# Kernel tuning notes

Hardware: AMD Instinct MI355X
Metric: run time of the kernel (lower is better)

Reference implementation:

```python
import jax, jax.numpy as jnp
import numpy as np

B, E, S, H, HD, M, MLP = 8, 1024, 2000, 16, 64, 10, 4096
EPS = 1e-5

def setup_inputs() -> dict:
    key = jax.random.key(0)
    ks = jax.random.split(key, 12)
    s = lambda k, shape, sc: jax.random.normal(k, shape, dtype=jnp.float32) * sc
    return {
        'X': s(ks[0], (B, E, S), 1.0),
        'Wq': s(ks[1], (H, HD, E), E ** -0.5), 'bq': s(ks[2], (H, HD), 0.02),
        'Wk': s(ks[3], (H, HD, E), E ** -0.5), 'bk': s(ks[4], (H, HD), 0.02),
        'Wv': s(ks[5], (H, HD, E), E ** -0.5), 'bv': s(ks[6], (H, HD), 0.02),
        'g1': jnp.ones((E,), jnp.float32), 'be1': jnp.zeros((E,), jnp.float32),
        'W1': s(ks[7], (MLP, E), E ** -0.5), 'b1': s(ks[8], (MLP,), 0.02),
        'W2': s(ks[9], (E, MLP), MLP ** -0.5), 'b2': s(ks[10], (E,), 0.02),
        'g2': jnp.ones((E,), jnp.float32), 'be2': jnp.zeros((E,), jnp.float32),
    }

def iterative_inv(K, n_iter=6):
    I = jnp.eye(K.shape[-1], dtype=K.dtype)
    # global (over all batch/head) max row-sum * max col-sum init, as in Nystromformer
    V = K.swapaxes(-1, -2) / (jnp.max(jnp.sum(jnp.abs(K), axis=-2)) * jnp.max(jnp.sum(jnp.abs(K), axis=-1)))
    for _ in range(n_iter):
        KV = K @ V
        V = 0.25 * V @ (13.0 * I - KV @ (15.0 * I - KV @ (7.0 * I - KV)))
    return V

def layer_norm(x, g, b):
    mu = jnp.mean(x, axis=-1, keepdims=True)
    var = jnp.var(x, axis=-1, keepdims=True)
    return (x - mu) * jax.lax.rsqrt(var + EPS) * g + b

def reference(X, Wq, bq, Wk, bk, Wv, bv, g1, be1, W1, b1, W2, b2, g2, be2):
    x = jnp.swapaxes(X, 1, 2)  # (B, S, E)
    # per-head projections (stacked): (B, H, S, HD)
    Q = jnp.einsum('bse,hde->bhsd', x, Wq) + bq[None, :, None, :]
    K = jnp.einsum('bse,hde->bhsd', x, Wk) + bk[None, :, None, :]
    V = jnp.einsum('bse,hde->bhsd', x, Wv) + bv[None, :, None, :]
    scale = 1.0 / np.sqrt(np.sqrt(HD)).astype(np.float32)
    Q = Q * scale
    K = K * scale
    # landmarks: mean over segments of length S//M -> (B, H, M, HD)
    Ql = Q.reshape(B, H, M, S // M, HD).mean(axis=-2)
    Kl = K.reshape(B, H, M, S // M, HD).mean(axis=-2)
    k1 = jax.nn.softmax(jnp.einsum('bhsd,bhmd->bhsm', Q, Kl), axis=-1)   # (B,H,S,M)
    k2 = jax.nn.softmax(jnp.einsum('bhnd,bhmd->bhnm', Ql, Kl), axis=-1)  # (B,H,M,M)
    k3 = jax.nn.softmax(jnp.einsum('bhmd,bhsd->bhms', Ql, K), axis=-1)   # (B,H,M,S)
    attn = (k1 @ iterative_inv(k2)) @ (k3 @ V)  # (B,H,S,HD)
    attn = jnp.swapaxes(attn, 1, 2).reshape(B, S, E)
    h = layer_norm(attn, g1, be1)
    h = jax.nn.gelu(h @ W1.T + b1, approximate=False)
    h = h @ W2.T + b2
    h = layer_norm(h, g2, be2)
    return jnp.swapaxes(h, 2, 1)  # (B, E, S)
```

## Files before the change

kernel.cpp:

```cpp
#include <hip/hip_runtime.h>
#include <cmath>
#include <cstdint>
#include <cstddef>

#define BB 8
#define EE 1024
#define SS 2000
#define HH 16
#define HDIM 64
#define MLM 10
#define MLPD 4096
#define QKV_N 3072
#define QK_SCALE 0.35355339059327373f

typedef __attribute__((ext_vector_type(8))) short short8v;
typedef __attribute__((ext_vector_type(4))) float f32x4;

static __device__ __forceinline__ short f2bf(float x) {
  unsigned u = __builtin_bit_cast(unsigned, x);
  unsigned r = (u + 0x7fffu + ((u >> 16) & 1u)) >> 16;
  return (short)(unsigned short)r;
}
static __device__ __forceinline__ float bf2f(short x) {
  unsigned u = ((unsigned)(unsigned short)x) << 16;
  return __builtin_bit_cast(float, u);
}

static __device__ __forceinline__ void load_lds16(const short* g, short* l) {
  __builtin_amdgcn_global_load_lds(
      (const __attribute__((address_space(1))) void*)g,
      (__attribute__((address_space(3))) void*)l, 16, 0, 0);
}

__global__ __launch_bounds__(256) void transpose_x(const float* __restrict__ X, short* __restrict__ xb) {
  __shared__ float tile[32][33];
  int b = blockIdx.z;
  int e0 = blockIdx.y * 32;
  int s0 = blockIdx.x * 32;
  int tx = threadIdx.x;
  int ty = threadIdx.y;
#pragma unroll
  for (int i = 0; i < 32; i += 8) {
    int e = e0 + ty + i, s = s0 + tx;
    tile[ty + i][tx] = (s < SS) ? X[((size_t)b * EE + e) * SS + s] : 0.f;
  }
  __syncthreads();
#pragma unroll
  for (int i = 0; i < 32; i += 8) {
    int s = s0 + ty + i, e = e0 + tx;
    if (s < SS) xb[((size_t)b * SS + s) * EE + e] = f2bf(tile[tx][ty + i]);
  }
}

__global__ __launch_bounds__(256) void cast_f2b(const float* __restrict__ src, short* __restrict__ dst, int n) {
  int i = blockIdx.x * 256 + threadIdx.x;
  int stride = gridDim.x * 256;
  for (; i < n; i += stride) dst[i] = f2bf(src[i]);
}

__global__ __launch_bounds__(256) void gemm_bt(
    const short* __restrict__ A, const short* __restrict__ Bm, void* __restrict__ Cv,
    int K, int N, int mode,
    const float* __restrict__ p0, const float* __restrict__ p1, const float* __restrict__ p2)
{
  __shared__ __align__(16) short As[128 * 32];
  __shared__ __align__(16) short Bs[128 * 32];
  int tid = threadIdx.x;
  int NT_N = N >> 7;
  int ntX = NT_N >> 3;
  int lin = blockIdx.x;
  int xcd = lin & 7;
  int idx = lin >> 3;
  int m0 = (idx / ntX) * 128;
  int n0 = (xcd * ntX + (idx % ntX)) * 128;

  int wave = tid >> 6, lane = tid & 63;
  int wm = (wave & 1) * 64, wn = (wave >> 1) * 64;
  int lm = lane & 15, quad = lane >> 4;
  int lrow = lane >> 2;
  int lcol = (lane & 3) << 3;
  const short* Ag0 = A + (size_t)(m0 + wave * 32 + lrow) * K + lcol;
  const short* Ag1 = Ag0 + (size_t)16 * K;
  const short* Bg0 = Bm + (size_t)(n0 + wave * 32 + lrow) * K + lcol;
  const short* Bg1 = Bg0 + (size_t)16 * K;
  short* Al0 = &As[(wave * 32) * 32];
  short* Al1 = &As[(wave * 32 + 16) * 32];
  short* Bl0 = &Bs[(wave * 32) * 32];
  short* Bl1 = &Bs[(wave * 32 + 16) * 32];

  f32x4 acc[4][4];
#pragma unroll
  for (int i = 0; i < 4; i++)
#pragma unroll
    for (int j = 0; j < 4; j++) acc[i][j] = (f32x4){0.f, 0.f, 0.f, 0.f};

  for (int k0 = 0; k0 < K; k0 += 32) {
    __syncthreads();
    load_lds16(Ag0 + k0, Al0);
    load_lds16(Ag1 + k0, Al1);
    load_lds16(Bg0 + k0, Bl0);
    load_lds16(Bg1 + k0, Bl1);
    __syncthreads();
    short8v af[4], bfr[4];
#pragma unroll
    for (int i = 0; i < 4; i++) af[i] = *(const short8v*)&As[(wm + i * 16 + lm) * 32 + quad * 8];
#pragma unroll
    for (int j = 0; j < 4; j++) bfr[j] = *(const short8v*)&Bs[(wn + j * 16 + lm) * 32 + quad * 8];
#pragma unroll
    for (int i = 0; i < 4; i++)
#pragma unroll
      for (int j = 0; j < 4; j++)
        acc[i][j] = __builtin_amdgcn_mfma_f32_16x16x32_bf16(af[i], bfr[j], acc[i][j], 0, 0, 0);
  }
#pragma unroll
  for (int i = 0; i < 4; i++) {
#pragma unroll
    for (int j = 0; j < 4; j++) {
      int col = n0 + wn + j * 16 + lm;
      float bias, scl = 1.f;
      if (mode == 0) {
        if (col < 1024)      { bias = p0[col];        scl = QK_SCALE; }
        else if (col < 2048) { bias = p1[col - 1024]; scl = QK_SCALE; }
        else                 { bias = p2[col - 2048]; }
      } else {
        bias = p0[col];
      }
#pragma unroll
      for (int r = 0; r < 4; r++) {
        int row = m0 + wm + i * 16 + quad * 4 + r;
        float v = acc[i][j][r] + bias;
        if (mode == 0)      v *= scl;
        else if (mode == 1) v = 0.5f * v * (1.f + erff(v * 0.70710678118f));
        if (mode == 2) ((float*)Cv)[(size_t)row * N + col] = v;
        else           ((short*)Cv)[(size_t)row * N + col] = f2bf(v);
      }
    }
  }
}

__global__ __launch_bounds__(64) void landmarks(const short* __restrict__ QKV, float* __restrict__ Ql, float* __restrict__ Kl) {
  int d = threadIdx.x;
  int bhm = blockIdx.x;
  int part = blockIdx.y;
  int b = bhm / (HH * MLM);
  int h = (bhm / MLM) % HH;
  int m = bhm % MLM;
  const short* src = QKV + (part ? 1024 : 0);
  size_t base = ((size_t)(b * SS + m * 200)) * QKV_N + h * HDIM + d;
  float acc = 0.f;
  for (int i = 0; i < 200; i++) acc += bf2f(src[base + (size_t)i * QKV_N]);
  float* dst = part ? Kl : Ql;
  dst[((size_t)(b * HH + h) * MLM + m) * HDIM + d] = acc * (1.f / 200.f);
}

__global__ __launch_bounds__(128) void k2stats(const float* __restrict__ Ql, const float* __restrict__ Kl,
                                               float* __restrict__ k2, float* __restrict__ cmax, float* __restrict__ rmax) {
  int bh = blockIdx.x;
  __shared__ float QlS[640], KlS[640], zz[100], k2s[100], cs[10], rs[10];
  for (int i = threadIdx.x; i < 640; i += 128) {
    QlS[i] = Ql[(size_t)bh * 640 + i];
    KlS[i] = Kl[(size_t)bh * 640 + i];
  }
  __syncthreads();
  if (threadIdx.x < 100) {
    int i = threadIdx.x / 10, j = threadIdx.x % 10;
    float z = 0.f;
    for (int d = 0; d < 64; d++) z += QlS[i * 64 + d] * KlS[j * 64 + d];
    zz[threadIdx.x] = z;
  }
  __syncthreads();
  if (threadIdx.x < 10) {
    int i = threadIdx.x;
    float mx = -1e30f;
    for (int j = 0; j < 10; j++) mx = fmaxf(mx, zz[i * 10 + j]);
    float s = 0.f, e[10];
    for (int j = 0; j < 10; j++) { e[j] = expf(zz[i * 10 + j] - mx); s += e[j]; }
    float inv = 1.f / s, rsum = 0.f;
    for (int j = 0; j < 10; j++) {
      float v = e[j] * inv;
      k2s[i * 10 + j] = v;
      k2[(size_t)bh * 100 + i * 10 + j] = v;
      rsum += v;
    }
    rs[i] = rsum;
  }
  __syncthreads();
  if (threadIdx.x < 10) {
    int j = threadIdx.x;
    float c = 0.f;
    for (int i = 0; i < 10; i++) c += k2s[i * 10 + j];
    cs[j] = c;
  }
  __syncthreads();
  if (threadIdx.x == 0) {
    float m1 = 0.f, m2 = 0.f;
    for (int j = 0; j < 10; j++) { m1 = fmaxf(m1, cs[j]); m2 = fmaxf(m2, rs[j]); }
    cmax[bh] = m1;
    rmax[bh] = m2;
  }
}

__global__ __launch_bounds__(128) void invk(const float* __restrict__ k2, const float* __restrict__ cmax,
                                            const float* __restrict__ rmax, float* __restrict__ invo) {
  int bh = blockIdx.x;
  __shared__ float gsc;
  __shared__ float Km[100], Vm[100], KV[100], Ta[100], Tb[100];
  if (threadIdx.x == 0) {
    float mc = 0.f, mr = 0.f;
    for (int i = 0; i < 128; i++) { mc = fmaxf(mc, cmax[i]); mr = fmaxf(mr, rmax[i]); }
    gsc = 1.f / (mc * mr);
  }
  for (int i = threadIdx.x; i < 100; i += 128) Km[i] = k2[(size_t)bh * 100 + i];
  __syncthreads();
  int t = threadIdx.x;
  int i = t / 10, j = t % 10;
  bool act = t < 100;
  if (act) Vm[t] = Km[j * 10 + i] * gsc;
  __syncthreads();
  for (int it = 0; it < 6; it++) {
    if (act) { float a = 0.f; for (int k = 0; k < 10; k++) a += Km[i * 10 + k] * Vm[k * 10 + j]; KV[t] = a; }
    __syncthreads();
    if (act) Ta[t] = (i == j ? 7.f : 0.f) - KV[t];
    __syncthreads();
    if (act) { float a = 0.f; for (int k = 0; k < 10; k++) a += KV[i * 10 + k] * Ta[k * 10 + j]; Tb[t] = (i == j ? 15.f : 0.f) - a; }
    __syncthreads();
    if (act) { float a = 0.f; for (int k = 0; k < 10; k++) a += KV[i * 10 + k] * Tb[k * 10 + j]; Ta[t] = (i == j ? 13.f : 0.f) - a; }
    __syncthreads();
    if (act) { float a = 0.f; for (int k = 0; k < 10; k++) a += Vm[i * 10 + k] * Ta[k * 10 + j]; Tb[t] = 0.25f * a; }
    __syncthreads();
    if (act) Vm[t] = Tb[t];
    __syncthreads();
  }
  if (act) invo[(size_t)bh * 100 + t] = Vm[t];
}

__global__ __launch_bounds__(256) void k1inv_kernel(const short* __restrict__ QKV, const float* __restrict__ Kl,
                                                    const float* __restrict__ invg, float* __restrict__ k1inv) {
  int b = blockIdx.y;
  int s0 = blockIdx.x * 16;
  __shared__ float KlS[16 * 650];
  __shared__ float invS[16 * 101];
  for (int idx = threadIdx.x; idx < 16 * 640; idx += 256) {
    int h = idx / 640, r = idx % 640;
    KlS[h * 650 + r] = Kl[(size_t)(b * HH + h) * 640 + r];
  }
  for (int idx = threadIdx.x; idx < 1600; idx += 256) {
    int h = idx / 100, r = idx % 100;
    invS[h * 101 + r] = invg[(size_t)(b * HH + h) * 100 + r];
  }
  __syncthreads();
  int sl = threadIdx.x >> 4, h = threadIdx.x & 15;
  int s = s0 + sl;
  size_t qoff = (size_t)(b * SS + s) * QKV_N + h * HDIM;
  float z[10];
#pragma unroll
  for (int m = 0; m < 10; m++) z[m] = 0.f;
  for (int c = 0; c < 8; c++) {
    short8v qv = *(const short8v*)&QKV[qoff + c * 8];
    float qf[8];
#pragma unroll
    for (int jj = 0; jj < 8; jj++) qf[jj] = bf2f(qv[jj]);
#pragma unroll
    for (int m = 0; m < 10; m++) {
      const float* kl = &KlS[h * 650 + m * 64 + c * 8];
      float a = 0.f;
#pragma unroll
      for (int jj = 0; jj < 8; jj++) a += qf[jj] * kl[jj];
      z[m] += a;
    }
  }
  float mx = z[0];
#pragma unroll
  for (int m = 1; m < 10; m++) mx = fmaxf(mx, z[m]);
  float p[10], ssum = 0.f;
#pragma unroll
  for (int m = 0; m < 10; m++) { p[m] = expf(z[m] - mx); ssum += p[m]; }
  float rinv = 1.f / ssum;
  float* dst = &k1inv[((size_t)(b * SS + s) * HH + h) * MLM];
#pragma unroll
  for (int mm = 0; mm < 10; mm++) {
    float a = 0.f;
#pragma unroll
    for (int jjj = 0; jjj < 10; jjj++) a += p[jjj] * invS[h * 101 + jjj * 10 + mm];
    dst[mm] = a * rinv;
  }
}

__global__ __launch_bounds__(256) void k3v_kernel(const short* __restrict__ QKV, const float* __restrict__ Qlg,
                                                  float* __restrict__ kvout) {
  int bh = blockIdx.x;
  int b = bh >> 4, h = bh & 15;
  __shared__ float Kt[64 * 65];
  __shared__ float Vt[64 * 65];
  __shared__ float eS[10 * 64];
  __shared__ float QlS[640];
  __shared__ float denS[10];
  int tid = threadIdx.x;
  int wave = tid >> 6, lane = tid & 63;
  for (int i = tid; i < 640; i += 256) QlS[i] = Qlg[(size_t)bh * 640 + i];
  float myden = 0.f;
  float accn[3] = {0.f, 0.f, 0.f};
  int rowi = tid >> 2;
  int d0 = (tid & 3) * 16;
  for (int s0 = 0; s0 < SS; s0 += 64) {
    __syncthreads();
    if (s0 + rowi < SS) {
      size_t base = (size_t)(b * SS + s0 + rowi) * QKV_N + h * HDIM + d0;
      short8v k0v = *(const short8v*)&QKV[base + 1024];
      short8v k1v = *(const short8v*)&QKV[base + 1024 + 8];
      short8v v0v = *(const short8v*)&QKV[base + 2048];
      short8v v1v = *(const short8v*)&QKV[base + 2048 + 8];
#pragma unroll
      for (int jj = 0; jj < 8; jj++) {
        Kt[rowi * 65 + d0 + jj]     = bf2f(k0v[jj]);
        Kt[rowi * 65 + d0 + 8 + jj] = bf2f(k1v[jj]);
        Vt[rowi * 65 + d0 + jj]     = bf2f(v0v[jj]);
        Vt[rowi * 65 + d0 + 8 + jj] = bf2f(v1v[jj]);
      }
    }
    __syncthreads();
    for (int mb = 0; mb < 12; mb += 4) {
      int m = mb + wave;
      if (m < 10) {
        float z = 0.f;
        const float* kr = &Kt[lane * 65];
        const float* ql = &QlS[m * 64];
        for (int d = 0; d < 64; d++) z += ql[d] * kr[d];
        eS[m * 64 + lane] = (s0 + lane < SS) ? expf(z) : 0.f;
      }
    }
    __syncthreads();
    if (tid < 10) {
      float a = 0.f;
      for (int slj = 0; slj < 64; slj++) a += eS[tid * 64 + slj];
      myden += a;
    }
#pragma unroll
    for (int ii = 0; ii < 3; ii++) {
      int idx = tid + ii * 256;
      if (idx < 640) {
        int m = idx >> 6, d = idx & 63;
        float a = 0.f;
        for (int slj = 0; slj < 64; slj++) a += eS[m * 64 + slj] * Vt[slj * 65 + d];
        accn[ii] += a;
      }
    }
  }
  if (tid < 10) denS[tid] = myden;
  __syncthreads();
#pragma unroll
  for (int ii = 0; ii < 3; ii++) {
    int idx = tid + ii * 256;
    if (idx < 640) {
      int m = idx >> 6;
      kvout[(size_t)bh * 640 + idx] = accn[ii] / denS[m];
    }
  }
}

__global__ __launch_bounds__(256) void attn_ln1(const float* __restrict__ k1inv, const float* __restrict__ kvg,
                                                const float* __restrict__ g1, const float* __restrict__ be1,
                                                short* __restrict__ h1) {
  int blk = blockIdx.x;
  int b = blk / SS;
  __shared__ float pS[160];
  __shared__ float red[8];
  for (int i = threadIdx.x; i < 160; i += 256) pS[i] = k1inv[(size_t)blk * 160 + i];
  __syncthreads();
  float vals[4], s1 = 0.f, s2 = 0.f;
#pragma unroll
  for (int i = 0; i < 4; i++) {
    int e = threadIdx.x + i * 256;
    int h = e >> 6, d = e & 63;
    const float* kvp = &kvg[((size_t)(b * HH + h) * MLM) * HDIM + d];
    const float* pp = &pS[h * 10];
    float a = 0.f;
#pragma unroll
    for (int m = 0; m < 10; m++) a += pp[m] * kvp[m * 64];
    vals[i] = a; s1 += a; s2 += a * a;
  }
#pragma unroll
  for (int off = 32; off; off >>= 1) { s1 += __shfl_down(s1, off); s2 += __shfl_down(s2, off); }
  int wv = threadIdx.x >> 6;
  if ((threadIdx.x & 63) == 0) { red[wv] = s1; red[4 + wv] = s2; }
  __syncthreads();
  float t1 = red[0] + red[1] + red[2] + red[3];
  float t2 = red[4] + red[5] + red[6] + red[7];
  float mean = t1 * (1.f / 1024.f);
  float var = t2 * (1.f / 1024.f) - mean * mean;
  float ninv = rsqrtf(var + 1e-5f);
#pragma unroll
  for (int i = 0; i < 4; i++) {
    int e = threadIdx.x + i * 256;
    h1[(size_t)blk * EE + e] = f2bf((vals[i] - mean) * ninv * g1[e] + be1[e]);
  }
}

__global__ __launch_bounds__(256) void ln2_kernel(const float* __restrict__ h2, const float* __restrict__ g2,
                                                  const float* __restrict__ be2, short* __restrict__ h3) {
  int blk = blockIdx.x;
  __shared__ float red[8];
  float vals[4], s1 = 0.f, s2 = 0.f;
#pragma unroll
  for (int i = 0; i < 4; i++) {
    int e = threadIdx.x + i * 256;
    float a = h2[(size_t)blk * EE + e];
    vals[i] = a; s1 += a; s2 += a * a;
  }
#pragma unroll
  for (int off = 32; off; off >>= 1) { s1 += __shfl_down(s1, off); s2 += __shfl_down(s2, off); }
  int wv = threadIdx.x >> 6;
  if ((threadIdx.x & 63) == 0) { red[wv] = s1; red[4 + wv] = s2; }
  __syncthreads();
  float t1 = red[0] + red[1] + red[2] + red[3];
  float t2 = red[4] + red[5] + red[6] + red[7];
  float mean = t1 * (1.f / 1024.f);
  float var = t2 * (1.f / 1024.f) - mean * mean;
  float ninv = rsqrtf(var + 1e-5f);
#pragma unroll
  for (int i = 0; i < 4; i++) {
    int e = threadIdx.x + i * 256;
    h3[(size_t)blk * EE + e] = f2bf((vals[i] - mean) * ninv * g2[e] + be2[e]);
  }
}

__global__ __launch_bounds__(256) void transpose_out(const short* __restrict__ h3, float* __restrict__ outp) {
  __shared__ short tile[64 * 65];
  int b = blockIdx.z;
  int e0 = blockIdx.y * 64;
  int s0 = blockIdx.x * 64;
  int tx = threadIdx.x & 63;
  int ty = threadIdx.x >> 6;
#pragma unroll
  for (int i = 0; i < 16; i++) {
    int r = ty + i * 4;
    int s = s0 + r;
    if (s < SS) tile[r * 65 + tx] = h3[((size_t)b * SS + s) * EE + e0 + tx];
  }
  __syncthreads();
#pragma unroll
  for (int i = 0; i < 16; i++) {
    int c = ty + i * 4;
    int s = s0 + tx;
    if (s < SS) outp[((size_t)b * EE + e0 + c) * SS + s] = bf2f(tile[tx * 65 + c]);
  }
}

#define ALIGN_UP(x) (((x) + 255) & ~(size_t)255)
static const size_t SZ_XB   = (size_t)BB * SS * EE * 2;
static const size_t SZ_WCAT = (size_t)QKV_N * EE * 2;
static const size_t SZ_W1B  = (size_t)MLPD * EE * 2;
static const size_t SZ_W2B  = (size_t)EE * MLPD * 2;
static const size_t SZ_QKV  = (size_t)BB * SS * QKV_N * 2;
static const int    CH0_NB  = 63, CH1_NB = 62;
static const size_t SZ_MID0 = (size_t)CH0_NB * 128 * MLPD * 2;
static const size_t SZ_H2_0 = (size_t)CH0_NB * 128 * EE * 4;
static const size_t SZ_SLOTB = (SZ_QKV > ALIGN_UP(SZ_MID0) + SZ_H2_0)
                               ? SZ_QKV : (ALIGN_UP(SZ_MID0) + SZ_H2_0);
static const size_t SZ_QL   = (size_t)BB * HH * MLM * HDIM * 4;
static const size_t SZ_K2   = (size_t)BB * HH * 100 * 4;
static const size_t SZ_ST   = 512;
static const size_t SZ_K1I  = (size_t)BB * SS * HH * MLM * 4;

extern "C" void kernel_launch(void* const* d_in, const int* in_sizes, int n_in,
                              void* d_out, int out_size, void* d_ws, size_t ws_size,
                              hipStream_t stream) {
  const float* X   = (const float*)d_in[0];
  const float* Wq  = (const float*)d_in[1];
  const float* bq  = (const float*)d_in[2];
  const float* Wk  = (const float*)d_in[3];
  const float* bk  = (const float*)d_in[4];
  const float* Wv  = (const float*)d_in[5];
  const float* bv  = (const float*)d_in[6];
  const float* g1  = (const float*)d_in[7];
  const float* be1 = (const float*)d_in[8];
  const float* W1  = (const float*)d_in[9];
  const float* b1  = (const float*)d_in[10];
  const float* W2  = (const float*)d_in[11];
  const float* b2  = (const float*)d_in[12];
  const float* g2  = (const float*)d_in[13];
  const float* be2 = (const float*)d_in[14];

  char* ws = (char*)d_ws;
  size_t off = 0;
  char* slotA = ws + off; off += ALIGN_UP(SZ_XB);
  char* slotB = ws + off; off += ALIGN_UP(SZ_SLOTB);
  char* slotC = ws + off; off += ALIGN_UP(SZ_XB);
  char* slotD = ws + off; off += ALIGN_UP(SZ_WCAT);
  short* W1b = (short*)(ws + off); off += ALIGN_UP(SZ_W1B);
  short* W2b = (short*)(ws + off); off += ALIGN_UP(SZ_W2B);
  float* k1ib = (float*)(ws + off); off += ALIGN_UP(SZ_K1I);

  short* xb   = (short*)slotA;
  short* h1   = (short*)slotA;
  short* qkv  = (short*)slotB;
  short* mid  = (short*)slotB;
  float* h2c  = (float*)(slotB + ALIGN_UP(SZ_MID0));
  short* h3   = (short*)slotC;
  short* Wcat = (short*)slotD;
  size_t doff = 0;
  float* Qlm  = (float*)(slotD + doff); doff += ALIGN_UP(SZ_QL);
  float* Klm  = (float*)(slotD + doff); doff += ALIGN_UP(SZ_QL);
  float* k2b  = (float*)(slotD + doff); doff += ALIGN_UP(SZ_K2);
  float* cmaxb= (float*)(slotD + doff); doff += ALIGN_UP(SZ_ST);
  float* rmaxb= (float*)(slotD + doff); doff += ALIGN_UP(SZ_ST);
  float* invb = (float*)(slotD + doff); doff += ALIGN_UP(SZ_K2);
  float* kvb  = (float*)(slotD + doff); doff += ALIGN_UP(SZ_QL);
  (void)ws_size; (void)in_sizes; (void)n_in; (void)out_size;

  transpose_x<<<dim3(63, 32, BB), dim3(32, 8), 0, stream>>>(X, xb);
  cast_f2b<<<2048, 256, 0, stream>>>(Wq, Wcat,             EE * EE);
  cast_f2b<<<2048, 256, 0, stream>>>(Wk, Wcat + EE * EE,   EE * EE);
  cast_f2b<<<2048, 256, 0, stream>>>(Wv, Wcat + 2*EE*EE,   EE * EE);
  cast_f2b<<<4096, 256, 0, stream>>>(W1, W1b, MLPD * EE);
  cast_f2b<<<4096, 256, 0, stream>>>(W2, W2b, EE * MLPD);
  gemm_bt<<<125 * 24, 256, 0, stream>>>(xb, Wcat, qkv, EE, QKV_N, 0, bq, bk, bv);
  landmarks<<<dim3(BB * HH * MLM, 2), 64, 0, stream>>>(qkv, Qlm, Klm);
  k2stats<<<BB * HH, 128, 0, stream>>>(Qlm, Klm, k2b, cmaxb, rmaxb);
  invk<<<BB * HH, 128, 0, stream>>>(k2b, cmaxb, rmaxb, invb);
  k1inv_kernel<<<dim3(125, BB), 256, 0, stream>>>(qkv, Klm, invb, k1ib);
  k3v_kernel<<<BB * HH, 256, 0, stream>>>(qkv, Qlm, kvb);
  attn_ln1<<<BB * SS, 256, 0, stream>>>(k1ib, kvb, g1, be1, h1);
  int row0 = 0;
  for (int c = 0; c < 2; c++) {
    int nb = (c == 0) ? CH0_NB : CH1_NB;
    int rows = nb * 128;
    gemm_bt<<<nb * 32, 256, 0, stream>>>(h1 + (size_t)row0 * EE, W1b, mid, EE, MLPD, 1, b1, nullptr, nullptr);
    gemm_bt<<<nb * 8,  256, 0, stream>>>(mid, W2b, h2c, MLPD, EE, 2, b2, nullptr, nullptr);
    ln2_kernel<<<rows, 256, 0, stream>>>(h2c, g2, be2, h3 + (size_t)row0 * EE);
    row0 += rows;
  }
  transpose_out<<<dim3(32, 16, BB), 256, 0, stream>>>(h3, (float*)d_out);
}
```

Measured before the change: 1.063 ms.

## Replace 128x128 GEMM with pipelined 256x256 tile kernel and unchunk MLP

Replaces the 128x128 single-buffered bf16 MFMA GEMM with a 512-thread 256x256-tile kernel. It double-buffers LDS with a swizzled layout, interleaves async global-to-LDS loads with MFMA phases, and uses setprio and explicit barriers. Rows are padded to 16128 so tiles divide evenly, and stores are masked. The MLP is no longer split into two chunks: the W2 fp32 output goes to the output buffer as scratch, and the workspace is reorganized. The goal is higher arithmetic intensity and load/compute overlap, at the cost of more LDS and register use and some padded work.

After: 1.047 ms. No clear change (-1.6%).

```diff
diff --git a/kernel.cpp b/kernel.cpp
--- a/kernel.cpp
+++ b/kernel.cpp
@@ -11,6 +11,7 @@
 #define MLM 10
 #define MLPD 4096
 #define QKV_N 3072
+#define MPAD 16128
 #define QK_SCALE 0.35355339059327373f
 
 typedef __attribute__((ext_vector_type(8))) short short8v;
@@ -58,84 +59,134 @@
   for (; i < n; i += stride) dst[i] = f2bf(src[i]);
 }
 
-__global__ __launch_bounds__(256) void gemm_bt(
+__global__ __launch_bounds__(512, 2) void gemm256(
     const short* __restrict__ A, const short* __restrict__ Bm, void* __restrict__ Cv,
-    int K, int N, int mode,
+    int K, int N, int mode, int Mstore,
     const float* __restrict__ p0, const float* __restrict__ p1, const float* __restrict__ p2)
 {
-  __shared__ __align__(16) short As[128 * 32];
-  __shared__ __align__(16) short Bs[128 * 32];
-  int tid = threadIdx.x;
-  int NT_N = N >> 7;
-  int ntX = NT_N >> 3;
-  int lin = blockIdx.x;
-  int xcd = lin & 7;
-  int idx = lin >> 3;
-  int m0 = (idx / ntX) * 128;
-  int n0 = (xcd * ntX + (idx % ntX)) * 128;
-
-  int wave = tid >> 6, lane = tid & 63;
-  int wm = (wave & 1) * 64, wn = (wave >> 1) * 64;
-  int lm = lane & 15, quad = lane >> 4;
-  int lrow = lane >> 2;
-  int lcol = (lane & 3) << 3;
-  const short* Ag0 = A + (size_t)(m0 + wave * 32 + lrow) * K + lcol;
-  const short* Ag1 = Ag0 + (size_t)16 * K;
-  const short* Bg0 = Bm + (size_t)(n0 + wave * 32 + lrow) * K + lcol;
-  const short* Bg1 = Bg0 + (size_t)16 * K;
-  short* Al0 = &As[(wave * 32) * 32];
-  short* Al1 = &As[(wave * 32 + 16) * 32];
-  short* Bl0 = &Bs[(wave * 32) * 32];
-  short* Bl1 = &Bs[(wave * 32 + 16) * 32];
-
-  f32x4 acc[4][4];
-#pragma unroll
-  for (int i = 0; i < 4; i++)
+  __shared__ __align__(16) short lds[65536];
+  const int tid = threadIdx.x;
+
+  const int NT_N = N >> 8;
+  const int NT_M = gridDim.x / NT_N;
+  const int per = NT_M << 2;
+  const int g4 = blockIdx.x / per;
+  const int rem = blockIdx.x % per;
+  const int n0 = (g4 * 4 + (rem & 3)) << 8;
+  const int m0 = (rem >> 2) << 8;
+
+  const int lane = tid & 63, wv = tid >> 6;
+  const int wm = wv >> 2, wn = wv & 3;
+  const int lm = lane & 15, quad = lane >> 4;
+  const int rslot = (quad ^ (lm >> 2)) & 3;
+  const int aoff = (wm * 128 + lm) * 32 + rslot * 8;
+  const int boff = (wn * 64 + lm) * 32 + rslot * 8;
+
+  const int srow = tid >> 2;
+  const int sslot = (tid & 3) ^ ((tid >> 4) & 3);
+  const short* Ag = A + (size_t)(m0 + srow) * K + sslot * 8;
+  const short* Bg = Bm + (size_t)(n0 + srow) * K + sslot * 8;
+  const int wofs = (tid >> 6) << 9;
+
+  f32x4 acc[8][4];
+#pragma unroll
+  for (int i = 0; i < 8; i++)
 #pragma unroll
     for (int j = 0; j < 4; j++) acc[i][j] = (f32x4){0.f, 0.f, 0.f, 0.f};
-
-  for (int k0 = 0; k0 < K; k0 += 32) {
-    __syncthreads();
-    load_lds16(Ag0 + k0, Al0);
-    load_lds16(Ag1 + k0, Al1);
-    load_lds16(Bg0 + k0, Bl0);
-    load_lds16(Bg1 + k0, Bl1);
-    __syncthreads();
-    short8v af[4], bfr[4];
-#pragma unroll
-    for (int i = 0; i < 4; i++) af[i] = *(const short8v*)&As[(wm + i * 16 + lm) * 32 + quad * 8];
-#pragma unroll
-    for (int j = 0; j < 4; j++) bfr[j] = *(const short8v*)&Bs[(wn + j * 16 + lm) * 32 + quad * 8];
-#pragma unroll
-    for (int i = 0; i < 4; i++)
-#pragma unroll
-      for (int j = 0; j < 4; j++)
-        acc[i][j] = __builtin_amdgcn_mfma_f32_16x16x32_bf16(af[i], bfr[j], acc[i][j], 0, 0, 0);
-  }
-#pragma unroll
-  for (int i = 0; i < 4; i++) {
-#pragma unroll
-    for (int j = 0; j < 4; j++) {
-      int col = n0 + wn + j * 16 + lm;
-      float bias, scl = 1.f;
-      if (mode == 0) {
-        if (col < 1024)      { bias = p0[col];        scl = QK_SCALE; }
-        else if (col < 2048) { bias = p1[col - 1024]; scl = QK_SCALE; }
-        else                 { bias = p2[col - 2048]; }
-      } else {
-        bias = p0[col];
+  short8v afr[8], bfr[4];
+
+#define RGN(buf, op, kh) (&lds[((((buf)*2 + (op)) * 2 + (kh)) << 13)])
+#define STG(op, buf, kh, kt) do {                                          \
+    const short* gp_ = ((op) ? Bg : Ag) + ((kt) * 64 + (kh) * 32);         \
+    short* lp_ = RGN(buf, op, kh) + wofs;                                  \
+    load_lds16(gp_, lp_);                                                  \
+    load_lds16(gp_ + (size_t)128 * K, lp_ + 4096);                         \
+  } while (0)
+#define LDA(buf, kh) do {                                                  \
+    const short* r_ = RGN(buf, 0, kh) + aoff;                              \
+    _Pragma("unroll") for (int i_ = 0; i_ < 8; ++i_)                       \
+      afr[i_] = *(const short8v*)(r_ + i_ * 512);                          \
+  } while (0)
+#define LDB(buf, kh, jb) do {                                              \
+    const short* r_ = RGN(buf, 1, kh) + boff;                              \
+    bfr[jb]     = *(const short8v*)(r_ + (jb) * 512);                      \
+    bfr[(jb)+1] = *(const short8v*)(r_ + ((jb)+1) * 512);                  \
+  } while (0)
+#define MM(jb) do {                                                        \
+    __builtin_amdgcn_s_setprio(1);                                         \
+    _Pragma("unroll") for (int i_ = 0; i_ < 8; ++i_) {                     \
+      acc[i_][jb]     = __builtin_amdgcn_mfma_f32_16x16x32_bf16(           \
+          afr[i_], bfr[jb],     acc[i_][jb],     0, 0, 0);                 \
+      acc[i_][(jb)+1] = __builtin_amdgcn_mfma_f32_16x16x32_bf16(           \
+          afr[i_], bfr[(jb)+1], acc[i_][(jb)+1], 0, 0, 0);                 \
+    }                                                                      \
+    __builtin_amdgcn_s_setprio(0);                                         \
+  } while (0)
+#define SBAR() do {                                                        \
+    __builtin_amdgcn_sched_barrier(0);                                     \
+    __builtin_amdgcn_s_barrier();                                          \
+    __builtin_amdgcn_sched_barrier(0);                                     \
+  } while (0)
+#define WAITV(n) asm volatile("s_waitcnt vmcnt(" #n ")" ::: "memory")
+
+#define ITER(it, LAST) do {                                                              \
+    LDB(0,0,0); LDA(0,0); STG(1,1,1, 2*(it)+1);                   SBAR(); MM(0); SBAR(); \
+    LDB(0,0,2);           if (!(LAST)) STG(0,0,0, 2*(it)+2);      SBAR(); MM(2); SBAR(); \
+    LDB(0,1,0); LDA(0,1); if (!(LAST)) STG(1,0,0, 2*(it)+2);      SBAR(); MM(0); SBAR(); \
+    LDB(0,1,2);           if (!(LAST)) { STG(0,0,1, 2*(it)+2); WAITV(6); }               \
+                          else         { WAITV(0); }              SBAR(); MM(2); SBAR(); \
+    LDB(1,0,0); LDA(1,0); if (!(LAST)) STG(1,0,1, 2*(it)+2);      SBAR(); MM(0); SBAR(); \
+    LDB(1,0,2);           if (!(LAST)) STG(0,1,0, 2*(it)+3);      SBAR(); MM(2); SBAR(); \
+    LDB(1,1,0); LDA(1,1); if (!(LAST)) STG(1,1,0, 2*(it)+3);      SBAR(); MM(0); SBAR(); \
+    LDB(1,1,2);           if (!(LAST)) { STG(0,1,1, 2*(it)+3); WAITV(6); }               \
+                                                                  SBAR(); MM(2); SBAR(); \
+  } while (0)
+
+  const int NI = K >> 7;
+  STG(0,0,0, 0); STG(1,0,0, 0); STG(0,0,1, 0); STG(1,0,1, 0);
+  STG(0,1,0, 1); STG(1,1,0, 1); STG(0,1,1, 1);
+  WAITV(6);
+  SBAR();
+
+  for (int it = 0; it < NI - 1; ++it) ITER(it, 0);
+  ITER(NI - 1, 1);
+
+  const int crow0 = m0 + wm * 128 + quad * 4;
+  const int ccol0 = n0 + wn * 64 + lm;
+#pragma unroll
+  for (int j = 0; j < 4; ++j) {
+    const int col = ccol0 + j * 16;
+    float bias, scl = 1.f;
+    if (mode == 0) {
+      if (col < 1024)      { bias = p0[col];        scl = QK_SCALE; }
+      else if (col < 2048) { bias = p1[col - 1024]; scl = QK_SCALE; }
+      else                 { bias = p2[col - 2048]; }
+    } else {
+      bias = p0[col];
+    }
+#pragma unroll
+    for (int i = 0; i < 8; ++i) {
+#pragma unroll
+      for (int r = 0; r < 4; ++r) {
+        const int row = crow0 + i * 16 + r;
+        if (row < Mstore) {
+          float v = acc[i][j][r] + bias;
+          if (mode == 0)      v *= scl;
+          else if (mode == 1) v = 0.5f * v * (1.f + erff(v * 0.70710678118f));
+          if (mode == 2) ((float*)Cv)[(size_t)row * N + col] = v;
+          else           ((short*)Cv)[(size_t)row * N + col] = f2bf(v);
+        }
       }
-#pragma unroll
-      for (int r = 0; r < 4; r++) {
-        int row = m0 + wm + i * 16 + quad * 4 + r;
-        float v = acc[i][j][r] + bias;
-        if (mode == 0)      v *= scl;
-        else if (mode == 1) v = 0.5f * v * (1.f + erff(v * 0.70710678118f));
-        if (mode == 2) ((float*)Cv)[(size_t)row * N + col] = v;
-        else           ((short*)Cv)[(size_t)row * N + col] = f2bf(v);
-      }
-    }
-  }
+    }
+  }
+#undef RGN
+#undef STG
+#undef LDA
+#undef LDB
+#undef MM
+#undef SBAR
+#undef WAITV
+#undef ITER
 }
 
 __global__ __launch_bounds__(64) void landmarks(const short* __restrict__ QKV, float* __restrict__ Ql, float* __restrict__ Kl) {
@@ -447,20 +498,15 @@
 }
 
 #define ALIGN_UP(x) (((x) + 255) & ~(size_t)255)
-static const size_t SZ_XB   = (size_t)BB * SS * EE * 2;
-static const size_t SZ_WCAT = (size_t)QKV_N * EE * 2;
-static const size_t SZ_W1B  = (size_t)MLPD * EE * 2;
-static const size_t SZ_W2B  = (size_t)EE * MLPD * 2;
-static const size_t SZ_QKV  = (size_t)BB * SS * QKV_N * 2;
-static const int    CH0_NB  = 63, CH1_NB = 62;
-static const size_t SZ_MID0 = (size_t)CH0_NB * 128 * MLPD * 2;
-static const size_t SZ_H2_0 = (size_t)CH0_NB * 128 * EE * 4;
-static const size_t SZ_SLOTB = (SZ_QKV > ALIGN_UP(SZ_MID0) + SZ_H2_0)
-                               ? SZ_QKV : (ALIGN_UP(SZ_MID0) + SZ_H2_0);
-static const size_t SZ_QL   = (size_t)BB * HH * MLM * HDIM * 4;
-static const size_t SZ_K2   = (size_t)BB * HH * 100 * 4;
-static const size_t SZ_ST   = 512;
-static const size_t SZ_K1I  = (size_t)BB * SS * HH * MLM * 4;
+static const size_t SZ_SLOTA = (size_t)MPAD * EE * 2;
+static const size_t SZ_QKV   = (size_t)MPAD * QKV_N * 2;
+static const size_t SZ_MID   = (size_t)MPAD * MLPD * 2;
+static const size_t SZ_WCAT  = (size_t)QKV_N * EE * 2;
+static const size_t SZ_W1B   = (size_t)MLPD * EE * 2;
+static const size_t SZ_W2B   = (size_t)EE * MLPD * 2;
+static const size_t SZ_QL    = (size_t)BB * HH * MLM * HDIM * 4;
+static const size_t SZ_K2    = (size_t)BB * HH * 100 * 4;
+static const size_t SZ_ST    = 512;
 
 extern "C" void kernel_launch(void* const* d_in, const int* in_sizes, int n_in,
                               void* d_out, int out_size, void* d_ws, size_t ws_size,
@@ -483,20 +529,18 @@
 
   char* ws = (char*)d_ws;
   size_t off = 0;
-  char* slotA = ws + off; off += ALIGN_UP(SZ_XB);
-  char* slotB = ws + off; off += ALIGN_UP(SZ_SLOTB);
-  char* slotC = ws + off; off += ALIGN_UP(SZ_XB);
+  char* slotA = ws + off; off += ALIGN_UP(SZ_SLOTA);
+  char* slotB = ws + off; off += ALIGN_UP(SZ_MID);
   char* slotD = ws + off; off += ALIGN_UP(SZ_WCAT);
   short* W1b = (short*)(ws + off); off += ALIGN_UP(SZ_W1B);
   short* W2b = (short*)(ws + off); off += ALIGN_UP(SZ_W2B);
-  float* k1ib = (float*)(ws + off); off += ALIGN_UP(SZ_K1I);
 
   short* xb   = (short*)slotA;
   short* h1   = (short*)slotA;
+  short* h3   = (short*)slotA;
   short* qkv  = (short*)slotB;
   short* mid  = (short*)slotB;
-  float* h2c  = (float*)(slotB + ALIGN_UP(SZ_MID0));
-  short* h3   = (short*)slotC;
+  float* k1ib = (float*)(slotB + ALIGN_UP(SZ_QKV));
   short* Wcat = (short*)slotD;
   size_t doff = 0;
   float* Qlm  = (float*)(slotD + doff); doff += ALIGN_UP(SZ_QL);
@@ -506,6 +550,7 @@
   float* rmaxb= (float*)(slotD + doff); doff += ALIGN_UP(SZ_ST);
   float* invb = (float*)(slotD + doff); doff += ALIGN_UP(SZ_K2);
   float* kvb  = (float*)(slotD + doff); doff += ALIGN_UP(SZ_QL);
+  float* h2c  = (float*)d_out;
   (void)ws_size; (void)in_sizes; (void)n_in; (void)out_size;
 
   transpose_x<<<dim3(63, 32, BB), dim3(32, 8), 0, stream>>>(X, xb);
@@ -514,21 +559,15 @@
   cast_f2b<<<2048, 256, 0, stream>>>(Wv, Wcat + 2*EE*EE,   EE * EE);
   cast_f2b<<<4096, 256, 0, stream>>>(W1, W1b, MLPD * EE);
   cast_f2b<<<4096, 256, 0, stream>>>(W2, W2b, EE * MLPD);
-  gemm_bt<<<125 * 24, 256, 0, stream>>>(xb, Wcat, qkv, EE, QKV_N, 0, bq, bk, bv);
+  gemm256<<<63 * 12, 512, 0, stream>>>(xb, Wcat, qkv, EE, QKV_N, 0, MPAD, bq, bk, bv);
   landmarks<<<dim3(BB * HH * MLM, 2), 64, 0, stream>>>(qkv, Qlm, Klm);
   k2stats<<<BB * HH, 128, 0, stream>>>(Qlm, Klm, k2b, cmaxb, rmaxb);
   invk<<<BB * HH, 128, 0, stream>>>(k2b, cmaxb, rmaxb, invb);
   k1inv_kernel<<<dim3(125, BB), 256, 0, stream>>>(qkv, Klm, invb, k1ib);
   k3v_kernel<<<BB * HH, 256, 0, stream>>>(qkv, Qlm, kvb);
   attn_ln1<<<BB * SS, 256, 0, stream>>>(k1ib, kvb, g1, be1, h1);
-  int row0 = 0;
-  for (int c = 0; c < 2; c++) {
-    int nb = (c == 0) ? CH0_NB : CH1_NB;
-    int rows = nb * 128;
-    gemm_bt<<<nb * 32, 256, 0, stream>>>(h1 + (size_t)row0 * EE, W1b, mid, EE, MLPD, 1, b1, nullptr, nullptr);
-    gemm_bt<<<nb * 8,  256, 0, stream>>>(mid, W2b, h2c, MLPD, EE, 2, b2, nullptr, nullptr);
-    ln2_kernel<<<rows, 256, 0, stream>>>(h2c, g2, be2, h3 + (size_t)row0 * EE);
-    row0 += rows;
-  }
+  gemm256<<<63 * 16, 512, 0, stream>>>(h1, W1b, mid, EE, MLPD, 1, MPAD, b1, nullptr, nullptr);
+  gemm256<<<63 * 4, 512, 0, stream>>>(mid, W2b, h2c, MLPD, EE, 2, BB * SS, b2, nullptr, nullptr);
+  ln2_kernel<<<BB * SS, 256, 0, stream>>>(h2c, g2, be2, h3);
   transpose_out<<<dim3(32, 16, BB), 256, 0, stream>>>(h3, (float*)d_out);
 }
```
